# Kernel optimization log

Hardware: AMD Instinct MI355X
Metric: run time of the kernel (lower is better)

## Reference

```python
import jax, jax.numpy as jnp
import numpy as np

B, N, D = 2, 2048, 1024
H = 16
HD = D // H
C = 4
INTERACTION_BOOST = 0.3
EPS = 1e-6


def _rmsnorm(t, w):
    # t: (B,H,N,HD), w: (HD,)
    var = jnp.mean(t * t, axis=-1, keepdims=True)
    return t * jax.lax.rsqrt(var + EPS) * w


def setup_inputs() -> dict:
    key = jax.random.key(0)
    ks = jax.random.split(key, 8)
    return {
        "x": jax.random.normal(ks[0], (B, N, D), dtype=jnp.float32),
        "character_masks": jax.random.uniform(ks[1], (B, C, N), dtype=jnp.float32),
        "interaction_mask": jax.random.uniform(ks[2], (B, N, N), dtype=jnp.float32),
        "W_qkv": jax.random.normal(ks[3], (3 * D, D), dtype=jnp.float32) * 0.02,
        "W_out": jax.random.normal(ks[4], (D, D), dtype=jnp.float32) * 0.02,
        "q_norm_w": jnp.ones((HD,), dtype=jnp.float32),
        "k_norm_w": jnp.ones((HD,), dtype=jnp.float32),
        "isolation_gate": jax.random.uniform(ks[5], (H,), dtype=jnp.float32),
    }


def reference(x, character_masks, interaction_mask, W_qkv, W_out,
              q_norm_w, k_norm_w, isolation_gate) -> jnp.ndarray:
    b, n, d = x.shape
    h, hd = isolation_gate.shape[0], d // isolation_gate.shape[0]

    qkv = x @ W_qkv.T                       # (B,N,3D)
    q, k, v = jnp.split(qkv, 3, axis=-1)
    def to_heads(t):
        return t.reshape(b, n, h, hd).transpose(0, 2, 1, 3)  # (B,H,N,HD)
    q, k, v = to_heads(q), to_heads(k), to_heads(v)

    q = _rmsnorm(q, q_norm_w)
    k = _rmsnorm(k, k_norm_w)

    scale = hd ** -0.5
    attn = jnp.einsum('bhqd,bhkd->bhqk', q, k) * scale   # (B,H,N,N)

    # isolation bias: same-character co-membership, row-max normalized
    same = jnp.einsum('bcq,bck->bqk', character_masks, character_masks)  # (B,N,N)
    same = same / jnp.clip(jnp.max(same, axis=-1, keepdims=True), 1e-6)
    bias = (same - 0.5) * 2.0 + INTERACTION_BOOST * interaction_mask     # (B,N,N)

    gate = jnp.clip(isolation_gate, 0.0, 1.0)[None, :, None, None]       # (1,H,1,1)
    attn = attn + gate * bias[:, None, :, :] * 3.0

    attn = jax.nn.softmax(attn, axis=-1)
    out = jnp.einsum('bhqk,bhkd->bhqd', attn, v)          # (B,H,N,HD)
    out = out.transpose(0, 2, 1, 3).reshape(b, n, d)      # (B,N,D)
    return out @ W_out.T
```

## Files before the change

kernel.cpp:

```cpp
#include <hip/hip_runtime.h>
#include <math.h>


typedef __attribute__((ext_vector_type(8))) short s8v;
typedef __attribute__((ext_vector_type(4))) short s4v;
typedef __attribute__((ext_vector_type(4))) float f4v;

#define L2E 1.44269504088896340736f

__device__ __forceinline__ unsigned short f2bf(float x) {
    union { float f; unsigned u; } v; v.f = x;
    unsigned r = v.u + 0x7FFF + ((v.u >> 16) & 1);
    return (unsigned short)(r >> 16);
}
__device__ __forceinline__ float bf2f(unsigned short h) {
    union { unsigned u; float f; } v; v.u = ((unsigned)h) << 16;
    return v.f;
}
__device__ __forceinline__ f4v mfma32(s8v a, s8v b, f4v c) {
    return __builtin_amdgcn_mfma_f32_16x16x32_bf16(a, b, c, 0, 0, 0);
}
__device__ __forceinline__ void gl_lds16(const void* g, void* l) {
    __builtin_amdgcn_global_load_lds(
        (const __attribute__((address_space(1))) unsigned*)g,
        (__attribute__((address_space(3))) unsigned*)l, 16, 0, 0);
}
__device__ __forceinline__ float exp2g(float x) {
    float r; asm("v_exp_f32 %0, %1" : "=v"(r) : "v"(x)); return r;
}

__global__ __launch_bounds__(256)
void planes_k(const float* __restrict__ src, short* __restrict__ ph,
              short* __restrict__ pl)
{
    const int i = blockIdx.x * 256 + threadIdx.x;
    float4 f = ((const float4*)src)[i];
    float fa[4] = {f.x, f.y, f.z, f.w};
    s4v h4, l4;
#pragma unroll
    for (int j = 0; j < 4; j++) {
        unsigned short hb = f2bf(fa[j]);
        h4[j] = (short)hb;
        l4[j] = (short)f2bf(fa[j] - bf2f(hb));
    }
    ((s4v*)ph)[i] = h4;
    ((s4v*)pl)[i] = l4;
}

template<int MODE, int TM>
__global__ __launch_bounds__(256, 3)
void gemm_mfma(const short* __restrict__ Ah, const short* __restrict__ Al,
               const short* __restrict__ Bh, const short* __restrict__ Bl,
               short* __restrict__ Qhp, short* __restrict__ Qlp,
               short* __restrict__ Khp, short* __restrict__ Klp,
               short* __restrict__ Vp, float* __restrict__ Cout,
               const float* __restrict__ qw, const float* __restrict__ kw)
{
    constexpr int MJ = (TM == 128) ? 4 : 2;
    constexpr int JW = (TM == 128) ? 64 : 32;
    __shared__ short sAh[TM*32], sAl[TM*32], sBh[128*32], sBl[128*32];

    const int t = threadIdx.x, w = t >> 6, lane = t & 63;
    const int col = lane & 15, quad = lane >> 4;
    const int wm = (TM == 128) ? (w >> 1) : 0;
    const int wn = (TM == 128) ? (w & 1) : w;
    const int m0 = blockIdx.y * TM, n0 = blockIdx.x * 128;

    f4v acc[4][MJ];
#pragma unroll
    for (int i = 0; i < 4; i++)
#pragma unroll
        for (int j = 0; j < MJ; j++) { f4v z = {0.f,0.f,0.f,0.f}; acc[i][j] = z; }

    const int r4 = lane >> 2;
    const int cs = ((lane & 3) ^ (r4 & 3)) * 8;
    const short* agh = Ah + (size_t)(m0 + w*16 + r4)*1024 + cs;
    const short* agl = Al + (size_t)(m0 + w*16 + r4)*1024 + cs;
    const short* bgh = Bh + (size_t)(n0 + w*16 + r4)*1024 + cs;
    const short* bgl = Bl + (size_t)(n0 + w*16 + r4)*1024 + cs;

    for (int kt = 0; kt < 32; kt++) {
        const int k0 = kt * 32;
        __syncthreads();
#pragma unroll
        for (int j = 0; j < TM/64; j++) {
            gl_lds16(agh + k0 + j*65536, &sAh[(j*4 + w)*512]);
            gl_lds16(agl + k0 + j*65536, &sAl[(j*4 + w)*512]);
        }
#pragma unroll
        for (int j = 0; j < 2; j++) {
            gl_lds16(bgh + k0 + j*65536, &sBh[(j*4 + w)*512]);
            gl_lds16(bgl + k0 + j*65536, &sBl[(j*4 + w)*512]);
        }
        __syncthreads();

        const int swz = ((quad ^ (col & 3)) << 3);
        s8v ahf[4], alf[4], bhf[MJ], blf[MJ];
#pragma unroll
        for (int i = 0; i < 4; i++) {
            const int aoff = (wm*64 + i*16 + col)*32 + swz;
            ahf[i] = *(const s8v*)&sAh[aoff];
            alf[i] = *(const s8v*)&sAl[aoff];
        }
#pragma unroll
        for (int j = 0; j < MJ; j++) {
            const int boff = (wn*JW + j*16 + col)*32 + swz;
            bhf[j] = *(const s8v*)&sBh[boff];
            blf[j] = *(const s8v*)&sBl[boff];
        }
#pragma unroll
        for (int i = 0; i < 4; i++)
#pragma unroll
        for (int j = 0; j < MJ; j++) {
            acc[i][j] = mfma32(ahf[i], bhf[j], acc[i][j]);
            acc[i][j] = mfma32(ahf[i], blf[j], acc[i][j]);
            acc[i][j] = mfma32(alf[i], bhf[j], acc[i][j]);
        }
    }

    if (MODE == 0) {
        const int whichW = (n0 + wn*64) >> 10;
        if (whichW < 2) {
            const float* nw = (whichW == 0) ? qw : kw;
            const float sfac = (whichW == 0) ? (0.125f * L2E) : 1.0f;
            float wj[4];
#pragma unroll
            for (int j = 0; j < 4; j++) wj[j] = nw[j*16 + col] * sfac;
#pragma unroll
            for (int i = 0; i < 4; i++)
#pragma unroll
            for (int r = 0; r < 4; r++) {
                float s2 = acc[i][0][r]*acc[i][0][r] + acc[i][1][r]*acc[i][1][r]
                         + acc[i][2][r]*acc[i][2][r] + acc[i][3][r]*acc[i][3][r];
                s2 += __shfl_xor(s2, 1);
                s2 += __shfl_xor(s2, 2);
                s2 += __shfl_xor(s2, 4);
                s2 += __shfl_xor(s2, 8);
                const float scn = rsqrtf(s2*(1.0f/64.0f) + 1e-6f);
#pragma unroll
                for (int j = 0; j < 4; j++) acc[i][j][r] *= scn*wj[j];
            }
        }
    }

    if (MODE == 0) {
#pragma unroll
        for (int i = 0; i < 4; i++)
#pragma unroll
        for (int j = 0; j < MJ; j++) {
            const int gcol = n0 + wn*JW + j*16 + col;
            const int which = gcol >> 10;
            const int hh = (gcol >> 6) & 15;
            const int hd = gcol & 63;
            const int grow0 = m0 + wm*64 + i*16 + quad*4;
            const int b = grow0 >> 11, nn0 = grow0 & 2047;
            if (which == 2) {
                s4v hv;
#pragma unroll
                for (int r = 0; r < 4; r++) hv[r] = (short)f2bf(acc[i][j][r]);
                const int nswz = (nn0 & ~60) | ((nn0 & 12) << 2) | ((nn0 & 48) >> 2);
                *(s4v*)&Vp[((size_t)(b*16 + hh)*64 + hd)*2048 + nswz] = hv;
            } else {
                short* Hp = (which == 0) ? Qhp : Khp;
                short* Lp = (which == 0) ? Qlp : Klp;
                const size_t base = ((size_t)(b*16 + hh)*2048 + nn0)*64 + hd;
#pragma unroll
                for (int r = 0; r < 4; r++) {
                    const float v = acc[i][j][r];
                    const unsigned short hb = f2bf(v);
                    union { float f; unsigned u; } rr; rr.f = v - bf2f(hb);
                    Hp[base + (size_t)r*64] = (short)hb;
                    Lp[base + (size_t)r*64] = (short)(rr.u >> 16);
                }
            }
        }
    } else {
#pragma unroll
        for (int i = 0; i < 4; i++)
#pragma unroll
        for (int j = 0; j < MJ; j++) {
            const int gcol = n0 + wn*JW + j*16 + col;
#pragma unroll
            for (int r = 0; r < 4; r++) {
                const int grow = m0 + wm*64 + i*16 + quad*4 + r;
                Cout[(size_t)grow*1024 + gcol] = acc[i][j][r];
            }
        }
    }
}

__global__ __launch_bounds__(256)
void rowscale_k(const float* __restrict__ cm, float* __restrict__ rs)
{
    __shared__ float cms[4][2048];
    const int b  = blockIdx.x >> 5;
    const int qt = blockIdx.x & 31;
    const float* base = cm + (size_t)b * 4 * 2048;
    for (int i = threadIdx.x; i < 2048; i += 256) {
        cms[0][i] = base[i];
        cms[1][i] = base[2048 + i];
        cms[2][i] = base[4096 + i];
        cms[3][i] = base[6144 + i];
    }
    __syncthreads();
    const int q    = qt * 64 + (threadIdx.x >> 2);
    const int part = threadIdx.x & 3;
    const float a0 = cms[0][q], a1 = cms[1][q], a2 = cms[2][q], a3 = cms[3][q];
    float mx = 0.f;
    for (int i = 0; i < 512; i++) {
        const int k = part + 4 * i;
        float d = a0*cms[0][k] + a1*cms[1][k] + a2*cms[2][k] + a3*cms[3][k];
        mx = fmaxf(mx, d);
    }
    mx = fmaxf(mx, __shfl_xor(mx, 1));
    mx = fmaxf(mx, __shfl_xor(mx, 2));
    if (part == 0) rs[b * 2048 + q] = 1.0f / fmaxf(mx, 1e-6f);
}

__global__ __launch_bounds__(256)
void bias_pre(const float* __restrict__ cm, const float* __restrict__ im,
              const float* __restrict__ rs, float* __restrict__ Bias2)
{
    const int bid = blockIdx.x;
    const int qq = bid & 3;
    const int kt = (bid >> 2) & 31;
    const int b  = bid >> 7;

    __shared__ float cmk[4][64];
    const int t = threadIdx.x;
    const int k0 = kt * 64;
    cmk[t >> 6][t & 63] = cm[(size_t)b*8192 + (t >> 6)*2048 + k0 + (t & 63)];
    __syncthreads();

    const int klane = t & 15;
    const int qrow  = t >> 4;
    const int kk = k0 + klane*4;
    const int kg = kk >> 2;
    float ck[4][4];
#pragma unroll
    for (int c = 0; c < 4; c++)
#pragma unroll
        for (int j = 0; j < 4; j++) ck[c][j] = cmk[c][klane*4 + j];

    const float* cmb = cm + (size_t)b * 8192;
    const float kS = 3.0f * L2E;
    for (int it = 0; it < 32; it++) {
        const int q = qq*512 + it*16 + qrow;
        float4 imv = *(const float4*)(im + ((size_t)b*2048 + q)*2048 + kk);
        const float rsq = rs[b*2048 + q];
        const float c0 = cmb[q], c1 = cmb[2048+q], c2 = cmb[4096+q], c3 = cmb[6144+q];
        float o[4];
        float iv[4] = {imv.x, imv.y, imv.z, imv.w};
#pragma unroll
        for (int j = 0; j < 4; j++) {
            float same = c0*ck[0][j] + c1*ck[1][j] + c2*ck[2][j] + c3*ck[3][j];
            o[j] = ((same*rsq - 0.5f)*2.0f + 0.3f*iv[j]) * kS;
        }
        *(float4*)(Bias2 + (((size_t)b*512 + kg)*2048 + q)*4) =
            make_float4(o[0], o[1], o[2], o[3]);
    }
}

__global__ __launch_bounds__(256, 2)
void attn_mfma(const short* __restrict__ Qhp, const short* __restrict__ Qlp,
               const short* __restrict__ Khg, const short* __restrict__ Klg,
               const short* __restrict__ VtG, const float* __restrict__ Bias2,
               const float* __restrict__ gate, short* __restrict__ Oh,
               short* __restrict__ Ol)
{
    const int bid = blockIdx.x;
    const int h  = bid & 15;
    const int qt = (bid >> 4) & 15;
    const int b  = bid >> 8;

    __shared__ __align__(16) short Kbuf[2][2][64*64];
    __shared__ __align__(16) short Vbuf[2][64*64];

    const int t    = threadIdx.x;
    const int w    = t >> 6;
    const int lane = t & 63;
    const int col  = lane & 15;
    const int quad = lane >> 4;

    const size_t headoff = ((size_t)(b*16 + h)) * 2048 * 64;
    const int qb = qt*128 + w*32;

    s8v qfh[2][2], qfl[2][2];
#pragma unroll
    for (int n = 0; n < 2; n++)
#pragma unroll
    for (int c = 0; c < 2; c++) {
        const size_t off = headoff + (size_t)(qb + n*16 + col)*64 + c*32 + quad*8;
        qfh[n][c] = *(const s8v*)(Qhp + off);
        qfl[n][c] = *(const s8v*)(Qlp + off);
    }

    const float g = fminf(fmaxf(gate[h], 0.f), 1.f);

    s8v ones8;
#pragma unroll
    for (int j = 0; j < 8; j++) ones8[j] = (short)0x3F80;

    f4v liacc[2];
    f4v Oa[4][2];
    {
        f4v z = {0.f,0.f,0.f,0.f};
        liacc[0] = z; liacc[1] = z;
#pragma unroll
        for (int dt = 0; dt < 4; dt++)
#pragma unroll
            for (int n = 0; n < 2; n++) Oa[dt][n] = z;
    }

    const short* ksrc_h = Khg + headoff + (size_t)(w*8 + (lane>>3))*64
                          + ((lane&7) ^ (lane>>3))*8;
    const short* ksrc_l = Klg + headoff + (size_t)(w*8 + (lane>>3))*64
                          + ((lane&7) ^ (lane>>3))*8;
    const short* vsrcT = VtG + headoff + (size_t)(w*8 + (lane>>3))*2048
                          + ((lane&7) ^ (lane>>3))*8;

    const float* bptr[2];
#pragma unroll
    for (int n = 0; n < 2; n++)
        bptr[n] = Bias2 + (((size_t)b*512 + quad)*2048 + qb + n*16 + col)*4;

    auto dma = [&](int kbase, int pp) {
#pragma unroll
        for (int j = 0; j < 2; j++) {
            gl_lds16(ksrc_h + (size_t)kbase*64 + j*2048, &Kbuf[pp][0][(j*4 + w)*512]);
            gl_lds16(ksrc_l + (size_t)kbase*64 + j*2048, &Kbuf[pp][1][(j*4 + w)*512]);
        }
#pragma unroll
        for (int cc = 0; cc < 2; cc++)
            gl_lds16(vsrcT + (size_t)(kbase + cc*65536), &Vbuf[pp][cc*2048 + w*512]);
    };

    float4 biasA[4][2], biasB[4][2];

    dma(0, 0);
#pragma unroll
    for (int s = 0; s < 4; s++)
#pragma unroll
    for (int n = 0; n < 2; n++)
        biasA[s][n] = *(const float4*)(bptr[n] + (size_t)s*4*8192);
    __syncthreads();

    auto tile = [&](int kt, int pp, float4 (&BC)[4][2], float4 (&BN)[4][2]) {
        const int kbase = kt * 64;
        const bool pre = kt < 31;
        if (pre) {
            dma(kbase + 64, pp ^ 1);
#pragma unroll
            for (int s = 0; s < 4; s++)
#pragma unroll
            for (int n = 0; n < 2; n++)
                BN[s][n] = *(const float4*)(bptr[n] +
                    ((size_t)((kbase >> 2) + 16) + s*4)*8192);
        }

        f4v S[4][2];
#pragma unroll
        for (int s = 0; s < 4; s++)
#pragma unroll
            for (int n = 0; n < 2; n++) { f4v z = {0.f,0.f,0.f,0.f}; S[s][n] = z; }
#pragma unroll
        for (int s = 0; s < 4; s++)
#pragma unroll
        for (int c = 0; c < 2; c++) {
            const int koff = (s*16 + col)*64 + (((c*4 + quad) ^ (col & 7)) << 3);
            s8v kh = *(const s8v*)&Kbuf[pp][0][koff];
            s8v kl = *(const s8v*)&Kbuf[pp][1][koff];
#pragma unroll
            for (int n = 0; n < 2; n++) {
                S[s][n] = mfma32(kh, qfh[n][c], S[s][n]);
                S[s][n] = mfma32(kh, qfl[n][c], S[s][n]);
                S[s][n] = mfma32(kl, qfh[n][c], S[s][n]);
            }
        }

        s8v ph8[2][2];
#pragma unroll
        for (int n = 0; n < 2; n++) {
            union { unsigned uu[4]; s8v v; } pk0, pk1;
#pragma unroll
            for (int s = 0; s < 4; s++) {
                const float bb[4] = {BC[s][n].x, BC[s][n].y, BC[s][n].z, BC[s][n].w};
                const float p0 = exp2g(fmaf(bb[0], g, S[s][n][0]));
                const float p1 = exp2g(fmaf(bb[1], g, S[s][n][1]));
                const float p2 = exp2g(fmaf(bb[2], g, S[s][n][2]));
                const float p3 = exp2g(fmaf(bb[3], g, S[s][n][3]));
                unsigned u01, u23;
                asm("v_cvt_pk_bf16_f32 %0, %1, %2" : "=v"(u01) : "v"(p0), "v"(p1));
                asm("v_cvt_pk_bf16_f32 %0, %1, %2" : "=v"(u23) : "v"(p2), "v"(p3));
                if (s < 2) { pk0.uu[s*2] = u01;     pk0.uu[s*2 + 1] = u23; }
                else       { pk1.uu[(s-2)*2] = u01; pk1.uu[(s-2)*2 + 1] = u23; }
            }
            ph8[n][0] = pk0.v;
            ph8[n][1] = pk1.v;
        }

#pragma unroll
        for (int n = 0; n < 2; n++)
#pragma unroll
        for (int m = 0; m < 2; m++)
            liacc[n] = mfma32(ones8, ph8[n][m], liacc[n]);

#pragma unroll
        for (int dt = 0; dt < 4; dt++) {
            const int vrow = (dt*16 + col)*64;
            s8v v0 = *(const s8v*)&Vbuf[pp][vrow + ((((quad*2)    ) ^ (col & 7)) << 3)];
            s8v v1 = *(const s8v*)&Vbuf[pp][vrow + ((((quad*2) + 1) ^ (col & 7)) << 3)];
#pragma unroll
            for (int n = 0; n < 2; n++) {
                Oa[dt][n] = mfma32(v0, ph8[n][0], Oa[dt][n]);
                Oa[dt][n] = mfma32(v1, ph8[n][1], Oa[dt][n]);
            }
        }

        if (pre) __syncthreads();
    };

    for (int kt = 0; kt < 32; kt += 2) {
        tile(kt,     0, biasA, biasB);
        tile(kt + 1, 1, biasB, biasA);
    }

#pragma unroll
    for (int n = 0; n < 2; n++) {
        const float inv = 1.0f / liacc[n][0];
        const size_t row = (size_t)b*2048 + qb + n*16 + col;
#pragma unroll
        for (int dt = 0; dt < 4; dt++) {
            s4v hv, lv;
#pragma unroll
            for (int r = 0; r < 4; r++) {
                float y = Oa[dt][n][r] * inv;
                unsigned short hb = f2bf(y);
                hv[r] = (short)hb;
                union { float f; unsigned u; } rr; rr.f = y - bf2f(hb);
                lv[r] = (short)(rr.u >> 16);
            }
            const size_t o = row*1024 + h*64 + dt*16 + quad*4;
            *(s4v*)&Oh[o] = hv;
            *(s4v*)&Ol[o] = lv;
        }
    }
}

extern "C" void kernel_launch(void* const* d_in, const int* in_sizes, int n_in,
                              void* d_out, int out_size, void* d_ws, size_t ws_size,
                              hipStream_t stream)
{
    const float* x    = (const float*)d_in[0];
    const float* cm   = (const float*)d_in[1];
    const float* im   = (const float*)d_in[2];
    const float* Wqkv = (const float*)d_in[3];
    const float* Wout = (const float*)d_in[4];
    const float* qw   = (const float*)d_in[5];
    const float* kw   = (const float*)d_in[6];
    const float* gate = (const float*)d_in[7];
    float* out = (float*)d_out;

    char* ws = (char*)d_ws;
    short* qhp = (short*)(ws);
    short* qlp = (short*)(ws +  8388608);
    short* khp = (short*)(ws + 16777216);
    short* klp = (short*)(ws + 25165824);
    short* vp  = (short*)(ws + 33554432);
    short* oh  = (short*)(ws + 41943040);
    short* ol  = (short*)(ws + 50331648);
    short* woh = (short*)(ws + 58720256);
    short* wol = (short*)(ws + 60817408);
    float* rsb = (float*)(ws + 62914560);
    char*  U   = ws + 62930944;
    short* xh  = (short*)(U);
    short* xl  = (short*)(U +  8388608);
    short* wqh = (short*)(U + 16777216);
    short* wql = (short*)(U + 23068672);
    float* bias2 = (float*)(U);

    planes_k<<<4096, 256, 0, stream>>>(x,    xh,  xl);
    planes_k<<<3072, 256, 0, stream>>>(Wqkv, wqh, wql);
    planes_k<<<1024, 256, 0, stream>>>(Wout, woh, wol);
    gemm_mfma<0,128><<<dim3(24, 32), 256, 0, stream>>>(xh, xl, wqh, wql,
        qhp, qlp, khp, klp, vp, nullptr, qw, kw);
    rowscale_k<<<64, 256, 0, stream>>>(cm, rsb);
    bias_pre<<<256, 256, 0, stream>>>(cm, im, rsb, bias2);
    attn_mfma<<<512, 256, 0, stream>>>(qhp, qlp, khp, klp, vp, bias2, gate,
                                       oh, ol);
    gemm_mfma<1,64><<<dim3(8, 64), 256, 0, stream>>>(oh, ol, woh, wol,
        nullptr, nullptr, nullptr, nullptr, nullptr, out, nullptr, nullptr);
}
```

Before: 354.6 us.

## Split QKV GEMM into a 256x256-tile double-buffered kernel

Gives the QKV projection its own kernel with 512 threads, 256x256 output tiles and a two-stage LDS double buffer, so the next K-slice is loaded while MFMAs run on the current one. Larger tiles raise operand reuse per LDS load and halve the barriers per K step. The cost is 128KB of dynamic LDS (one block per CU), much higher register pressure from 32 accumulator fragments per wave, and only 192 blocks, which may not fill all CUs evenly. The output projection keeps the old path as a separate specialised kernel.

Result: no change. 351.5 us (-0.9%).

```diff
diff --git a/kernel.cpp b/kernel.cpp
--- a/kernel.cpp
+++ b/kernel.cpp
@@ -47,30 +47,31 @@
     ((s4v*)pl)[i] = l4;
 }
 
-template<int MODE, int TM>
-__global__ __launch_bounds__(256, 3)
-void gemm_mfma(const short* __restrict__ Ah, const short* __restrict__ Al,
-               const short* __restrict__ Bh, const short* __restrict__ Bl,
-               short* __restrict__ Qhp, short* __restrict__ Qlp,
-               short* __restrict__ Khp, short* __restrict__ Klp,
-               short* __restrict__ Vp, float* __restrict__ Cout,
-               const float* __restrict__ qw, const float* __restrict__ kw)
-{
-    constexpr int MJ = (TM == 128) ? 4 : 2;
-    constexpr int JW = (TM == 128) ? 64 : 32;
-    __shared__ short sAh[TM*32], sAl[TM*32], sBh[128*32], sBl[128*32];
+__global__ __launch_bounds__(512, 2)
+void gemm_qkv(const short* __restrict__ Ah, const short* __restrict__ Al,
+              const short* __restrict__ Bh, const short* __restrict__ Bl,
+              short* __restrict__ Qhp, short* __restrict__ Qlp,
+              short* __restrict__ Khp, short* __restrict__ Klp,
+              short* __restrict__ Vp,
+              const float* __restrict__ qw, const float* __restrict__ kw)
+{
+    extern __shared__ short L[];
+    short* sAh = L;
+    short* sAl = L + 16384;
+    short* sBh = L + 32768;
+    short* sBl = L + 49152;
 
     const int t = threadIdx.x, w = t >> 6, lane = t & 63;
     const int col = lane & 15, quad = lane >> 4;
-    const int wm = (TM == 128) ? (w >> 1) : 0;
-    const int wn = (TM == 128) ? (w & 1) : w;
-    const int m0 = blockIdx.y * TM, n0 = blockIdx.x * 128;
-
-    f4v acc[4][MJ];
-#pragma unroll
-    for (int i = 0; i < 4; i++)
-#pragma unroll
-        for (int j = 0; j < MJ; j++) { f4v z = {0.f,0.f,0.f,0.f}; acc[i][j] = z; }
+    const int wm = w >> 2;
+    const int wn = w & 3;
+    const int m0 = blockIdx.y * 256, n0 = blockIdx.x * 256;
+
+    f4v acc[8][4];
+#pragma unroll
+    for (int i = 0; i < 8; i++)
+#pragma unroll
+        for (int j = 0; j < 4; j++) { f4v z = {0.f,0.f,0.f,0.f}; acc[i][j] = z; }
 
     const int r4 = lane >> 2;
     const int cs = ((lane & 3) ^ (r4 & 3)) * 8;
@@ -79,6 +80,131 @@
     const short* bgh = Bh + (size_t)(n0 + w*16 + r4)*1024 + cs;
     const short* bgl = Bl + (size_t)(n0 + w*16 + r4)*1024 + cs;
 
+    auto stage = [&](int k0, int pp) {
+        const int dbase = pp*8192 + w*512;
+#pragma unroll
+        for (int j = 0; j < 2; j++) {
+            gl_lds16(agh + k0 + j*131072, &sAh[dbase + j*4096]);
+            gl_lds16(agl + k0 + j*131072, &sAl[dbase + j*4096]);
+            gl_lds16(bgh + k0 + j*131072, &sBh[dbase + j*4096]);
+            gl_lds16(bgl + k0 + j*131072, &sBl[dbase + j*4096]);
+        }
+    };
+
+    stage(0, 0);
+    __syncthreads();
+
+    for (int kt = 0; kt < 32; kt++) {
+        const int pp = kt & 1;
+        if (kt < 31) stage((kt + 1) * 32, pp ^ 1);
+
+        const int swz = ((quad ^ (col & 3)) << 3);
+        s8v bhf[4], blf[4];
+#pragma unroll
+        for (int j = 0; j < 4; j++) {
+            const int boff = pp*8192 + (wn*64 + j*16 + col)*32 + swz;
+            bhf[j] = *(const s8v*)&sBh[boff];
+            blf[j] = *(const s8v*)&sBl[boff];
+        }
+#pragma unroll
+        for (int i = 0; i < 8; i++) {
+            const int aoff = pp*8192 + (wm*128 + i*16 + col)*32 + swz;
+            s8v ah = *(const s8v*)&sAh[aoff];
+            s8v al = *(const s8v*)&sAl[aoff];
+#pragma unroll
+            for (int j = 0; j < 4; j++) {
+                acc[i][j] = mfma32(ah, bhf[j], acc[i][j]);
+                acc[i][j] = mfma32(ah, blf[j], acc[i][j]);
+                acc[i][j] = mfma32(al, bhf[j], acc[i][j]);
+            }
+        }
+        __syncthreads();
+    }
+
+    const int whichW = (n0 + wn*64) >> 10;
+    if (whichW < 2) {
+        const float* nw = (whichW == 0) ? qw : kw;
+        const float sfac = (whichW == 0) ? (0.125f * L2E) : 1.0f;
+        float wj[4];
+#pragma unroll
+        for (int j = 0; j < 4; j++) wj[j] = nw[j*16 + col] * sfac;
+#pragma unroll
+        for (int i = 0; i < 8; i++)
+#pragma unroll
+        for (int r = 0; r < 4; r++) {
+            float s2 = acc[i][0][r]*acc[i][0][r] + acc[i][1][r]*acc[i][1][r]
+                     + acc[i][2][r]*acc[i][2][r] + acc[i][3][r]*acc[i][3][r];
+            s2 += __shfl_xor(s2, 1);
+            s2 += __shfl_xor(s2, 2);
+            s2 += __shfl_xor(s2, 4);
+            s2 += __shfl_xor(s2, 8);
+            const float scn = rsqrtf(s2*(1.0f/64.0f) + 1e-6f);
+#pragma unroll
+            for (int j = 0; j < 4; j++) acc[i][j][r] *= scn*wj[j];
+        }
+    }
+
+#pragma unroll
+    for (int i = 0; i < 8; i++)
+#pragma unroll
+    for (int j = 0; j < 4; j++) {
+        const int gcol = n0 + wn*64 + j*16 + col;
+        const int which = gcol >> 10;
+        const int hh = (gcol >> 6) & 15;
+        const int hd = gcol & 63;
+        const int grow0 = m0 + wm*128 + i*16 + quad*4;
+        const int b = grow0 >> 11, nn0 = grow0 & 2047;
+        if (which == 2) {
+            s4v hv;
+#pragma unroll
+            for (int r = 0; r < 4; r++) hv[r] = (short)f2bf(acc[i][j][r]);
+            const int nswz = (nn0 & ~60) | ((nn0 & 12) << 2) | ((nn0 & 48) >> 2);
+            *(s4v*)&Vp[((size_t)(b*16 + hh)*64 + hd)*2048 + nswz] = hv;
+        } else {
+            short* Hp = (which == 0) ? Qhp : Khp;
+            short* Lp = (which == 0) ? Qlp : Klp;
+            const size_t base = ((size_t)(b*16 + hh)*2048 + nn0)*64 + hd;
+#pragma unroll
+            for (int r = 0; r < 4; r++) {
+                const float v = acc[i][j][r];
+                const unsigned short hb = f2bf(v);
+                union { float f; unsigned u; } rr; rr.f = v - bf2f(hb);
+                Hp[base + (size_t)r*64] = (short)hb;
+                Lp[base + (size_t)r*64] = (short)(rr.u >> 16);
+            }
+        }
+    }
+}
+
+template<int TM>
+__global__ __launch_bounds__(256, 3)
+void gemm_out(const short* __restrict__ Ah, const short* __restrict__ Al,
+              const short* __restrict__ Bh, const short* __restrict__ Bl,
+              float* __restrict__ Cout)
+{
+    constexpr int MJ = 2;
+    constexpr int JW = 32;
+    __shared__ short sAh[TM*32], sAl[TM*32], sBh[128*32], sBl[128*32];
+
+    const int t = threadIdx.x, w = t >> 6, lane = t & 63;
+    const int col = lane & 15, quad = lane >> 4;
+    const int wm = 0;
+    const int wn = w;
+    const int m0 = blockIdx.y * TM, n0 = blockIdx.x * 128;
+
+    f4v acc[4][MJ];
+#pragma unroll
+    for (int i = 0; i < 4; i++)
+#pragma unroll
+        for (int j = 0; j < MJ; j++) { f4v z = {0.f,0.f,0.f,0.f}; acc[i][j] = z; }
+
+    const int r4 = lane >> 2;
+    const int cs = ((lane & 3) ^ (r4 & 3)) * 8;
+    const short* agh = Ah + (size_t)(m0 + w*16 + r4)*1024 + cs;
+    const short* agl = Al + (size_t)(m0 + w*16 + r4)*1024 + cs;
+    const short* bgh = Bh + (size_t)(n0 + w*16 + r4)*1024 + cs;
+    const short* bgl = Bl + (size_t)(n0 + w*16 + r4)*1024 + cs;
+
     for (int kt = 0; kt < 32; kt++) {
         const int k0 = kt * 32;
         __syncthreads();
@@ -118,73 +244,15 @@
         }
     }
 
-    if (MODE == 0) {
-        const int whichW = (n0 + wn*64) >> 10;
-        if (whichW < 2) {
-            const float* nw = (whichW == 0) ? qw : kw;
-            const float sfac = (whichW == 0) ? (0.125f * L2E) : 1.0f;
-            float wj[4];
-#pragma unroll
-            for (int j = 0; j < 4; j++) wj[j] = nw[j*16 + col] * sfac;
-#pragma unroll
-            for (int i = 0; i < 4; i++)
-#pragma unroll
-            for (int r = 0; r < 4; r++) {
-                float s2 = acc[i][0][r]*acc[i][0][r] + acc[i][1][r]*acc[i][1][r]
-                         + acc[i][2][r]*acc[i][2][r] + acc[i][3][r]*acc[i][3][r];
-                s2 += __shfl_xor(s2, 1);
-                s2 += __shfl_xor(s2, 2);
-                s2 += __shfl_xor(s2, 4);
-                s2 += __shfl_xor(s2, 8);
-                const float scn = rsqrtf(s2*(1.0f/64.0f) + 1e-6f);
-#pragma unroll
-                for (int j = 0; j < 4; j++) acc[i][j][r] *= scn*wj[j];
-            }
-        }
-    }
-
-    if (MODE == 0) {
-#pragma unroll
-        for (int i = 0; i < 4; i++)
-#pragma unroll
-        for (int j = 0; j < MJ; j++) {
-            const int gcol = n0 + wn*JW + j*16 + col;
-            const int which = gcol >> 10;
-            const int hh = (gcol >> 6) & 15;
-            const int hd = gcol & 63;
-            const int grow0 = m0 + wm*64 + i*16 + quad*4;
-            const int b = grow0 >> 11, nn0 = grow0 & 2047;
-            if (which == 2) {
-                s4v hv;
-#pragma unroll
-                for (int r = 0; r < 4; r++) hv[r] = (short)f2bf(acc[i][j][r]);
-                const int nswz = (nn0 & ~60) | ((nn0 & 12) << 2) | ((nn0 & 48) >> 2);
-                *(s4v*)&Vp[((size_t)(b*16 + hh)*64 + hd)*2048 + nswz] = hv;
-            } else {
-                short* Hp = (which == 0) ? Qhp : Khp;
-                short* Lp = (which == 0) ? Qlp : Klp;
-                const size_t base = ((size_t)(b*16 + hh)*2048 + nn0)*64 + hd;
-#pragma unroll
-                for (int r = 0; r < 4; r++) {
-                    const float v = acc[i][j][r];
-                    const unsigned short hb = f2bf(v);
-                    union { float f; unsigned u; } rr; rr.f = v - bf2f(hb);
-                    Hp[base + (size_t)r*64] = (short)hb;
-                    Lp[base + (size_t)r*64] = (short)(rr.u >> 16);
-                }
-            }
-        }
-    } else {
-#pragma unroll
-        for (int i = 0; i < 4; i++)
-#pragma unroll
-        for (int j = 0; j < MJ; j++) {
-            const int gcol = n0 + wn*JW + j*16 + col;
-#pragma unroll
-            for (int r = 0; r < 4; r++) {
-                const int grow = m0 + wm*64 + i*16 + quad*4 + r;
-                Cout[(size_t)grow*1024 + gcol] = acc[i][j][r];
-            }
+#pragma unroll
+    for (int i = 0; i < 4; i++)
+#pragma unroll
+    for (int j = 0; j < MJ; j++) {
+        const int gcol = n0 + wn*JW + j*16 + col;
+#pragma unroll
+        for (int r = 0; r < 4; r++) {
+            const int grow = m0 + wm*64 + i*16 + quad*4 + r;
+            Cout[(size_t)grow*1024 + gcol] = acc[i][j][r];
         }
     }
 }
@@ -479,15 +547,21 @@
     short* wql = (short*)(U + 23068672);
     float* bias2 = (float*)(U);
 
+    static bool lds_init = false;
+    if (!lds_init) {
+        hipFuncSetAttribute((const void*)gemm_qkv,
+                            hipFuncAttributeMaxDynamicSharedMemorySize, 131072);
+        lds_init = true;
+    }
+
     planes_k<<<4096, 256, 0, stream>>>(x,    xh,  xl);
     planes_k<<<3072, 256, 0, stream>>>(Wqkv, wqh, wql);
     planes_k<<<1024, 256, 0, stream>>>(Wout, woh, wol);
-    gemm_mfma<0,128><<<dim3(24, 32), 256, 0, stream>>>(xh, xl, wqh, wql,
-        qhp, qlp, khp, klp, vp, nullptr, qw, kw);
+    gemm_qkv<<<dim3(12, 16), 512, 131072, stream>>>(xh, xl, wqh, wql,
+        qhp, qlp, khp, klp, vp, qw, kw);
     rowscale_k<<<64, 256, 0, stream>>>(cm, rsb);
     bias_pre<<<256, 256, 0, stream>>>(cm, im, rsb, bias2);
     attn_mfma<<<512, 256, 0, stream>>>(qhp, qlp, khp, klp, vp, bias2, gate,
                                        oh, ol);
-    gemm_mfma<1,64><<<dim3(8, 64), 256, 0, stream>>>(oh, ol, woh, wol,
-        nullptr, nullptr, nullptr, nullptr, nullptr, out, nullptr, nullptr);
-}
+    gemm_out<64><<<dim3(8, 64), 256, 0, stream>>>(oh, ol, woh, wol, out);
+}
```

## Rewrite projection GEMMs with double-buffered LDS, 512-thread blocks and persistent tiles

Applied to the files above, without the earlier changes.

Replaces the split-bf16 MFMA GEMM with a 512-thread, 128x128-tile kernel. It double-buffers LDS through async global-to-LDS loads so the next K-slice loads while the current one computes. The QKV GEMM becomes persistent, with each of 256 blocks looping over three output tiles and prefetching the next tile's first slice during the epilogue. The bias precompute grid is also split into four times more, smaller blocks to raise parallelism. The trade-offs are more LDS per block (64 KB dynamic), fewer resident waves, and reliance on barriers to order the async LDS loads correctly.

New measurement: 351.0 us. Within noise of the previous version (-1.0%).

```diff
diff --git a/kernel.cpp b/kernel.cpp
--- a/kernel.cpp
+++ b/kernel.cpp
@@ -47,143 +47,156 @@
     ((s4v*)pl)[i] = l4;
 }
 
-template<int MODE, int TM>
-__global__ __launch_bounds__(256, 3)
-void gemm_mfma(const short* __restrict__ Ah, const short* __restrict__ Al,
-               const short* __restrict__ Bh, const short* __restrict__ Bl,
-               short* __restrict__ Qhp, short* __restrict__ Qlp,
-               short* __restrict__ Khp, short* __restrict__ Klp,
-               short* __restrict__ Vp, float* __restrict__ Cout,
-               const float* __restrict__ qw, const float* __restrict__ kw)
+template<int MODE, int NT>
+__global__ __launch_bounds__(512, 2)
+void gemm2(const short* __restrict__ Ah, const short* __restrict__ Al,
+           const short* __restrict__ Bh, const short* __restrict__ Bl,
+           short* __restrict__ Qhp, short* __restrict__ Qlp,
+           short* __restrict__ Khp, short* __restrict__ Klp,
+           short* __restrict__ Vp, float* __restrict__ Cout,
+           const float* __restrict__ qw, const float* __restrict__ kw)
 {
-    constexpr int MJ = (TM == 128) ? 4 : 2;
-    constexpr int JW = (TM == 128) ? 64 : 32;
-    __shared__ short sAh[TM*32], sAl[TM*32], sBh[128*32], sBl[128*32];
+    extern __shared__ short L[];
+    short* sAh = L;
+    short* sAl = L + 8192;
+    short* sBh = L + 16384;
+    short* sBl = L + 24576;
 
     const int t = threadIdx.x, w = t >> 6, lane = t & 63;
     const int col = lane & 15, quad = lane >> 4;
-    const int wm = (TM == 128) ? (w >> 1) : 0;
-    const int wn = (TM == 128) ? (w & 1) : w;
-    const int m0 = blockIdx.y * TM, n0 = blockIdx.x * 128;
-
-    f4v acc[4][MJ];
-#pragma unroll
-    for (int i = 0; i < 4; i++)
-#pragma unroll
-        for (int j = 0; j < MJ; j++) { f4v z = {0.f,0.f,0.f,0.f}; acc[i][j] = z; }
-
-    const int r4 = lane >> 2;
-    const int cs = ((lane & 3) ^ (r4 & 3)) * 8;
-    const short* agh = Ah + (size_t)(m0 + w*16 + r4)*1024 + cs;
-    const short* agl = Al + (size_t)(m0 + w*16 + r4)*1024 + cs;
-    const short* bgh = Bh + (size_t)(n0 + w*16 + r4)*1024 + cs;
-    const short* bgl = Bl + (size_t)(n0 + w*16 + r4)*1024 + cs;
-
-    for (int kt = 0; kt < 32; kt++) {
-        const int k0 = kt * 32;
+    const int wm = w >> 1;
+    const int wn = w & 1;
+
+    const int srow = t >> 2;
+    const int sko  = ((t & 3) ^ (srow & 3)) * 8;
+    const int sdst = t * 8;
+
+    int tid = blockIdx.x;
+    int m0 = (tid & 31) * 128, n0 = (tid >> 5) * 128;
+    const short* agh = Ah + (size_t)(m0 + srow)*1024 + sko;
+    const short* agl = Al + (size_t)(m0 + srow)*1024 + sko;
+    const short* bgh = Bh + (size_t)(n0 + srow)*1024 + sko;
+    const short* bgl = Bl + (size_t)(n0 + srow)*1024 + sko;
+
+    auto stage = [&](int k0, int pp) {
+        gl_lds16(agh + k0, &sAh[pp*4096 + sdst]);
+        gl_lds16(agl + k0, &sAl[pp*4096 + sdst]);
+        gl_lds16(bgh + k0, &sBh[pp*4096 + sdst]);
+        gl_lds16(bgl + k0, &sBl[pp*4096 + sdst]);
+    };
+    stage(0, 0);
+
+    for (int rep = 0; rep < NT; rep++) {
         __syncthreads();
-#pragma unroll
-        for (int j = 0; j < TM/64; j++) {
-            gl_lds16(agh + k0 + j*65536, &sAh[(j*4 + w)*512]);
-            gl_lds16(agl + k0 + j*65536, &sAl[(j*4 + w)*512]);
-        }
-#pragma unroll
-        for (int j = 0; j < 2; j++) {
-            gl_lds16(bgh + k0 + j*65536, &sBh[(j*4 + w)*512]);
-            gl_lds16(bgl + k0 + j*65536, &sBl[(j*4 + w)*512]);
-        }
-        __syncthreads();
-
-        const int swz = ((quad ^ (col & 3)) << 3);
-        s8v ahf[4], alf[4], bhf[MJ], blf[MJ];
-#pragma unroll
-        for (int i = 0; i < 4; i++) {
-            const int aoff = (wm*64 + i*16 + col)*32 + swz;
-            ahf[i] = *(const s8v*)&sAh[aoff];
-            alf[i] = *(const s8v*)&sAl[aoff];
-        }
-#pragma unroll
-        for (int j = 0; j < MJ; j++) {
-            const int boff = (wn*JW + j*16 + col)*32 + swz;
-            bhf[j] = *(const s8v*)&sBh[boff];
-            blf[j] = *(const s8v*)&sBl[boff];
-        }
-#pragma unroll
-        for (int i = 0; i < 4; i++)
-#pragma unroll
-        for (int j = 0; j < MJ; j++) {
-            acc[i][j] = mfma32(ahf[i], bhf[j], acc[i][j]);
-            acc[i][j] = mfma32(ahf[i], blf[j], acc[i][j]);
-            acc[i][j] = mfma32(alf[i], bhf[j], acc[i][j]);
-        }
-    }
-
-    if (MODE == 0) {
-        const int whichW = (n0 + wn*64) >> 10;
-        if (whichW < 2) {
-            const float* nw = (whichW == 0) ? qw : kw;
-            const float sfac = (whichW == 0) ? (0.125f * L2E) : 1.0f;
-            float wj[4];
-#pragma unroll
-            for (int j = 0; j < 4; j++) wj[j] = nw[j*16 + col] * sfac;
-#pragma unroll
-            for (int i = 0; i < 4; i++)
-#pragma unroll
-            for (int r = 0; r < 4; r++) {
-                float s2 = acc[i][0][r]*acc[i][0][r] + acc[i][1][r]*acc[i][1][r]
-                         + acc[i][2][r]*acc[i][2][r] + acc[i][3][r]*acc[i][3][r];
-                s2 += __shfl_xor(s2, 1);
-                s2 += __shfl_xor(s2, 2);
-                s2 += __shfl_xor(s2, 4);
-                s2 += __shfl_xor(s2, 8);
-                const float scn = rsqrtf(s2*(1.0f/64.0f) + 1e-6f);
-#pragma unroll
-                for (int j = 0; j < 4; j++) acc[i][j][r] *= scn*wj[j];
-            }
-        }
-    }
-
-    if (MODE == 0) {
-#pragma unroll
-        for (int i = 0; i < 4; i++)
-#pragma unroll
-        for (int j = 0; j < MJ; j++) {
-            const int gcol = n0 + wn*JW + j*16 + col;
-            const int which = gcol >> 10;
-            const int hh = (gcol >> 6) & 15;
-            const int hd = gcol & 63;
-            const int grow0 = m0 + wm*64 + i*16 + quad*4;
-            const int b = grow0 >> 11, nn0 = grow0 & 2047;
-            if (which == 2) {
-                s4v hv;
-#pragma unroll
-                for (int r = 0; r < 4; r++) hv[r] = (short)f2bf(acc[i][j][r]);
-                const int nswz = (nn0 & ~60) | ((nn0 & 12) << 2) | ((nn0 & 48) >> 2);
-                *(s4v*)&Vp[((size_t)(b*16 + hh)*64 + hd)*2048 + nswz] = hv;
-            } else {
-                short* Hp = (which == 0) ? Qhp : Khp;
-                short* Lp = (which == 0) ? Qlp : Klp;
-                const size_t base = ((size_t)(b*16 + hh)*2048 + nn0)*64 + hd;
+
+        f4v acc[2][4];
+#pragma unroll
+        for (int i = 0; i < 2; i++)
+#pragma unroll
+            for (int j = 0; j < 4; j++) { f4v z = {0.f,0.f,0.f,0.f}; acc[i][j] = z; }
+
+        for (int kt = 0; kt < 32; kt++) {
+            const int pp = kt & 1;
+            if (kt < 31) stage((kt + 1) * 32, pp ^ 1);
+
+            const int swz = ((quad ^ (col & 3)) << 3);
+            s8v bhf[4], blf[4];
+#pragma unroll
+            for (int j = 0; j < 4; j++) {
+                const int boff = pp*4096 + (wn*64 + j*16 + col)*32 + swz;
+                bhf[j] = *(const s8v*)&sBh[boff];
+                blf[j] = *(const s8v*)&sBl[boff];
+            }
+#pragma unroll
+            for (int i = 0; i < 2; i++) {
+                const int aoff = pp*4096 + (wm*32 + i*16 + col)*32 + swz;
+                s8v ah = *(const s8v*)&sAh[aoff];
+                s8v al = *(const s8v*)&sAl[aoff];
+#pragma unroll
+                for (int j = 0; j < 4; j++) {
+                    acc[i][j] = mfma32(ah, bhf[j], acc[i][j]);
+                    acc[i][j] = mfma32(ah, blf[j], acc[i][j]);
+                    acc[i][j] = mfma32(al, bhf[j], acc[i][j]);
+                }
+            }
+            __syncthreads();
+        }
+
+        const int em0 = m0, en0 = n0;
+        if (rep + 1 < NT) {
+            tid = blockIdx.x + (rep + 1) * 256;
+            m0 = (tid & 31) * 128; n0 = (tid >> 5) * 128;
+            agh = Ah + (size_t)(m0 + srow)*1024 + sko;
+            agl = Al + (size_t)(m0 + srow)*1024 + sko;
+            bgh = Bh + (size_t)(n0 + srow)*1024 + sko;
+            bgl = Bl + (size_t)(n0 + srow)*1024 + sko;
+            stage(0, 0);
+        }
+
+        if (MODE == 0) {
+            const int whichW = (en0 + wn*64) >> 10;
+            if (whichW < 2) {
+                const float* nw = (whichW == 0) ? qw : kw;
+                const float sfac = (whichW == 0) ? (0.125f * L2E) : 1.0f;
+                float wj[4];
+#pragma unroll
+                for (int j = 0; j < 4; j++) wj[j] = nw[j*16 + col] * sfac;
+#pragma unroll
+                for (int i = 0; i < 2; i++)
 #pragma unroll
                 for (int r = 0; r < 4; r++) {
-                    const float v = acc[i][j][r];
-                    const unsigned short hb = f2bf(v);
-                    union { float f; unsigned u; } rr; rr.f = v - bf2f(hb);
-                    Hp[base + (size_t)r*64] = (short)hb;
-                    Lp[base + (size_t)r*64] = (short)(rr.u >> 16);
+                    float s2 = acc[i][0][r]*acc[i][0][r] + acc[i][1][r]*acc[i][1][r]
+                             + acc[i][2][r]*acc[i][2][r] + acc[i][3][r]*acc[i][3][r];
+                    s2 += __shfl_xor(s2, 1);
+                    s2 += __shfl_xor(s2, 2);
+                    s2 += __shfl_xor(s2, 4);
+                    s2 += __shfl_xor(s2, 8);
+                    const float scn = rsqrtf(s2*(1.0f/64.0f) + 1e-6f);
+#pragma unroll
+                    for (int j = 0; j < 4; j++) acc[i][j][r] *= scn*wj[j];
                 }
             }
-        }
-    } else {
-#pragma unroll
-        for (int i = 0; i < 4; i++)
-#pragma unroll
-        for (int j = 0; j < MJ; j++) {
-            const int gcol = n0 + wn*JW + j*16 + col;
-#pragma unroll
-            for (int r = 0; r < 4; r++) {
-                const int grow = m0 + wm*64 + i*16 + quad*4 + r;
-                Cout[(size_t)grow*1024 + gcol] = acc[i][j][r];
+#pragma unroll
+            for (int i = 0; i < 2; i++)
+#pragma unroll
+            for (int j = 0; j < 4; j++) {
+                const int gcol = en0 + wn*64 + j*16 + col;
+                const int which = gcol >> 10;
+                const int hh = (gcol >> 6) & 15;
+                const int hd = gcol & 63;
+                const int grow0 = em0 + wm*32 + i*16 + quad*4;
+                const int b = grow0 >> 11, nn0 = grow0 & 2047;
+                if (which == 2) {
+                    s4v hv;
+#pragma unroll
+                    for (int r = 0; r < 4; r++) hv[r] = (short)f2bf(acc[i][j][r]);
+                    const int nswz = (nn0 & ~60) | ((nn0 & 12) << 2) | ((nn0 & 48) >> 2);
+                    *(s4v*)&Vp[((size_t)(b*16 + hh)*64 + hd)*2048 + nswz] = hv;
+                } else {
+                    short* Hp = (which == 0) ? Qhp : Khp;
+                    short* Lp = (which == 0) ? Qlp : Klp;
+                    const size_t base = ((size_t)(b*16 + hh)*2048 + nn0)*64 + hd;
+#pragma unroll
+                    for (int r = 0; r < 4; r++) {
+                        const float v = acc[i][j][r];
+                        const unsigned short hb = f2bf(v);
+                        union { float f; unsigned u; } rr; rr.f = v - bf2f(hb);
+                        Hp[base + (size_t)r*64] = (short)hb;
+                        Lp[base + (size_t)r*64] = (short)(rr.u >> 16);
+                    }
+                }
+            }
+        } else {
+#pragma unroll
+            for (int i = 0; i < 2; i++)
+#pragma unroll
+            for (int j = 0; j < 4; j++) {
+                const int gcol = en0 + wn*64 + j*16 + col;
+#pragma unroll
+                for (int r = 0; r < 4; r++) {
+                    const int grow = em0 + wm*32 + i*16 + quad*4 + r;
+                    Cout[(size_t)grow*1024 + gcol] = acc[i][j][r];
+                }
             }
         }
     }
@@ -222,9 +235,9 @@
               const float* __restrict__ rs, float* __restrict__ Bias2)
 {
     const int bid = blockIdx.x;
-    const int qq = bid & 3;
-    const int kt = (bid >> 2) & 31;
-    const int b  = bid >> 7;
+    const int qq = bid & 15;
+    const int kt = (bid >> 4) & 31;
+    const int b  = bid >> 9;
 
     __shared__ float cmk[4][64];
     const int t = threadIdx.x;
@@ -244,8 +257,8 @@
 
     const float* cmb = cm + (size_t)b * 8192;
     const float kS = 3.0f * L2E;
-    for (int it = 0; it < 32; it++) {
-        const int q = qq*512 + it*16 + qrow;
+    for (int it = 0; it < 8; it++) {
+        const int q = qq*128 + it*16 + qrow;
         float4 imv = *(const float4*)(im + ((size_t)b*2048 + q)*2048 + kk);
         const float rsq = rs[b*2048 + q];
         const float c0 = cmb[q], c1 = cmb[2048+q], c2 = cmb[4096+q], c3 = cmb[6144+q];
@@ -479,15 +492,24 @@
     short* wql = (short*)(U + 23068672);
     float* bias2 = (float*)(U);
 
+    static bool lds_init = false;
+    if (!lds_init) {
+        hipFuncSetAttribute((const void*)&gemm2<0,3>,
+                            hipFuncAttributeMaxDynamicSharedMemorySize, 65536);
+        hipFuncSetAttribute((const void*)&gemm2<1,1>,
+                            hipFuncAttributeMaxDynamicSharedMemorySize, 65536);
+        lds_init = true;
+    }
+
     planes_k<<<4096, 256, 0, stream>>>(x,    xh,  xl);
     planes_k<<<3072, 256, 0, stream>>>(Wqkv, wqh, wql);
     planes_k<<<1024, 256, 0, stream>>>(Wout, woh, wol);
-    gemm_mfma<0,128><<<dim3(24, 32), 256, 0, stream>>>(xh, xl, wqh, wql,
+    gemm2<0,3><<<256, 512, 65536, stream>>>(xh, xl, wqh, wql,
         qhp, qlp, khp, klp, vp, nullptr, qw, kw);
     rowscale_k<<<64, 256, 0, stream>>>(cm, rsb);
-    bias_pre<<<256, 256, 0, stream>>>(cm, im, rsb, bias2);
+    bias_pre<<<1024, 256, 0, stream>>>(cm, im, rsb, bias2);
     attn_mfma<<<512, 256, 0, stream>>>(qhp, qlp, khp, klp, vp, bias2, gate,
                                        oh, ol);
-    gemm_mfma<1,64><<<dim3(8, 64), 256, 0, stream>>>(oh, ol, woh, wol,
+    gemm2<1,1><<<256, 512, 65536, stream>>>(oh, ol, woh, wol,
         nullptr, nullptr, nullptr, nullptr, nullptr, out, nullptr, nullptr);
 }
```
